# Optimization experiments

Measured on AMD Instinct MI355X. Metric: run time of the kernel, lower is better.

Reference implementation:

```python
import jax, jax.numpy as jnp
import numpy as np

D_IN = 4096
FEATURES = 4096
BATCH = 4096
NUM_ACTIVE = 50
ACTIVE_VAL = 3.0


def _sparse_init(key, shape, num_active=NUM_ACTIVE, active_val=ACTIVE_VAL):
    # Per output column: num_active inputs start ON (active_val), rest OFF (-3.0)
    scores = jax.random.uniform(key, shape)
    k = min(num_active, shape[0])
    threshold = jnp.sort(scores, axis=0)[-k]
    return jnp.where(scores >= threshold[None, :], active_val, -3.0).astype(jnp.float32)


def setup_inputs() -> dict:
    key = jax.random.key(0)
    kx, kw = jax.random.split(key)
    x = jax.random.normal(kx, (BATCH, D_IN), dtype=jnp.float32)
    w_raw = _sparse_init(kw, (D_IN, FEATURES))
    return {"x": x, "w_raw": w_raw}


def reference(x, w_raw):
    # Binary weights via straight-through estimator.
    w_soft = jax.nn.sigmoid(w_raw)
    w_hard = (w_raw > 0.0).astype(jnp.float32)
    w = w_soft + jax.lax.stop_gradient(w_hard - w_soft)
    return x @ w
```

## Files before the change

### kernel.cpp

```cpp
#include <hip/hip_runtime.h>
#include <hip/hip_fp16.h>

#define D_IN 4096
#define FEAT 4096
#define BATCH 4096
#define MAX_SLOTS 64
#define BFEAT 16
#define RCAP 8
#define OVCAP 16

typedef _Float16 h2 __attribute__((ext_vector_type(2)));

__device__ __forceinline__ h2 bc(unsigned u) { return __builtin_bit_cast(h2, u); }

__global__ void scan_kernel(const float* __restrict__ w,
                            unsigned int* __restrict__ c16,
                            unsigned char* __restrict__ rbuf,
                            unsigned int* __restrict__ ocnt,
                            unsigned short* __restrict__ ovf) {
    int t = blockIdx.x * blockDim.x + threadIdx.x;
    float4 v = ((const float4*)w)[t];
    int flat = t * 4;
    float a[4] = {v.x, v.y, v.z, v.w};
#pragma unroll
    for (int c = 0; c < 4; ++c) {
        if (a[c] > 0.0f) {
            int e = flat + c;
            int F = e & (FEAT - 1);
            int i = e >> 12;
            int r = i & 15;
            unsigned int p = atomicAdd(&c16[(F << 4) + r], 1u);
            if (p < RCAP) {
                rbuf[(size_t)((F << 4) + r) * RCAP + p] = (unsigned char)(i >> 4);
            } else {
                unsigned int op = atomicAdd(&ocnt[F], 1u);
                if (op < OVCAP) ovf[(size_t)F * OVCAP + op] = (unsigned short)i;
            }
        }
    }
}

__global__ __launch_bounds__(256)
void emit_kernel(const unsigned int* __restrict__ c16,
                 const unsigned char* __restrict__ rbuf,
                 const unsigned int* __restrict__ ocnt,
                 const unsigned short* __restrict__ ovf,
                 unsigned int* __restrict__ cnt,
                 unsigned short* __restrict__ idx) {
    __shared__ __align__(16) unsigned short outl[BFEAT][MAX_SLOTS];
    __shared__ unsigned short extras[BFEAT][48];
    __shared__ unsigned int   ecnt[BFEAT];
    __shared__ unsigned short kk[BFEAT][16];
    __shared__ unsigned short nn[BFEAT];

    const int tid = threadIdx.x;
    const int f0  = blockIdx.x * BFEAT;
    const int f   = tid >> 4, r = tid & 15;
    const int F   = f0 + f;

    if (tid < BFEAT) ecnt[tid] = 0u;
    __syncthreads();

    unsigned int c = c16[(F << 4) + r];
    int kr = c > RCAP ? RCAP : (int)c;
    kk[f][r] = (unsigned short)kr;
    __syncthreads();

    if (r == 0) {
        int s = 0;
#pragma unroll
        for (int q = 0; q < 16; ++q) s += (int)kk[f][q];
        int ov = (int)ocnt[F]; if (ov > OVCAP) ov = OVCAP;
        s += ov;
        if (s > MAX_SLOTS) s = MAX_SLOTS;
        nn[f] = (unsigned short)s;
        cnt[F] = (unsigned int)s;
    }
    __syncthreads();

    const int n = (int)nn[f];
    uint2 braw = *reinterpret_cast<const uint2*>(rbuf + (size_t)((F << 4) + r) * RCAP);
    const unsigned char* bs = reinterpret_cast<const unsigned char*>(&braw);
    const int base = (r - F) & 15;
    const int tgt  = (n >> 4) + (base < (n & 15) ? 1 : 0);
    const int m    = kr < tgt ? kr : tgt;
    for (int j = 0; j < m; ++j)
        outl[f][base + (j << 4)] = (unsigned short)(((int)bs[j] << 8) | (r << 4));
    for (int j = m; j < kr; ++j) {
        unsigned int e = atomicAdd(&ecnt[f], 1u);
        if (e < 48) extras[f][e] = (unsigned short)(((int)bs[j] << 8) | (r << 4));
    }
    if (r == 0) {
        int ov = (int)ocnt[F]; if (ov > OVCAP) ov = OVCAP;
        for (int j = 0; j < ov; ++j) {
            unsigned int e = atomicAdd(&ecnt[f], 1u);
            if (e < 48) extras[f][e] = (unsigned short)(ovf[(size_t)F * OVCAP + j] << 4);
        }
    }
    __syncthreads();

    if (tid < BFEAT) {
        const int ff = tid, FF = f0 + ff;
        const int n2 = (int)nn[ff];
        int ep = 0, ec = (int)ecnt[ff]; if (ec > 48) ec = 48;
        for (int r2 = 0; r2 < 16 && ep < ec; ++r2) {
            const int b2 = (r2 - FF) & 15;
            const int t2 = (n2 >> 4) + (b2 < (n2 & 15) ? 1 : 0);
            for (int j = (int)kk[ff][r2]; j < t2 && ep < ec; ++j)
                outl[ff][b2 + (j << 4)] = extras[ff][ep++];
        }
    }
    __syncthreads();

    if (tid < BFEAT * 8) {
        const int ff = tid >> 3, o = tid & 7;
        const uint4 v = *reinterpret_cast<const uint4*>(&outl[ff][o << 3]);
        reinterpret_cast<uint4*>(idx)[(size_t)o * FEAT + f0 + ff] = v;
    }
}

__device__ __forceinline__ void do_oct(uint4 p, const char* __restrict__ xtb,
                                       h2& A01, h2& A23, h2& A45, h2& A67,
                                       h2& B01, h2& B23, h2& B45, h2& B67) {
    uint4 v0 = *(const uint4*)(xtb + (p.x & 0xFFF0u));
    uint4 v1 = *(const uint4*)(xtb + (p.x >> 16));
    uint4 v2 = *(const uint4*)(xtb + (p.y & 0xFFF0u));
    uint4 v3 = *(const uint4*)(xtb + (p.y >> 16));
    uint4 v4 = *(const uint4*)(xtb + (p.z & 0xFFF0u));
    uint4 v5 = *(const uint4*)(xtb + (p.z >> 16));
    uint4 v6 = *(const uint4*)(xtb + (p.w & 0xFFF0u));
    uint4 v7 = *(const uint4*)(xtb + (p.w >> 16));
    A01 += bc(v0.x); A23 += bc(v0.y); A45 += bc(v0.z); A67 += bc(v0.w);
    B01 += bc(v1.x); B23 += bc(v1.y); B45 += bc(v1.z); B67 += bc(v1.w);
    A01 += bc(v2.x); A23 += bc(v2.y); A45 += bc(v2.z); A67 += bc(v2.w);
    B01 += bc(v3.x); B23 += bc(v3.y); B45 += bc(v3.z); B67 += bc(v3.w);
    A01 += bc(v4.x); A23 += bc(v4.y); A45 += bc(v4.z); A67 += bc(v4.w);
    B01 += bc(v5.x); B23 += bc(v5.y); B45 += bc(v5.z); B67 += bc(v5.w);
    A01 += bc(v6.x); A23 += bc(v6.y); A45 += bc(v6.z); A67 += bc(v6.w);
    B01 += bc(v7.x); B23 += bc(v7.y); B45 += bc(v7.z); B67 += bc(v7.w);
}

__global__ __launch_bounds__(1024, 8)
void gather_kernel(const float* __restrict__ x,
                   const unsigned int* __restrict__ cnt,
                   const uint4* __restrict__ q,
                   const unsigned short* __restrict__ q16,
                   float* __restrict__ out) {
    __shared__ uint4 xt[D_IN];
    const int tid = threadIdx.x;
    const int b0  = blockIdx.x * 8;
    const float* xb = x + (size_t)b0 * D_IN;

    for (int c = tid; c < D_IN; c += 1024) {
        float r0 = xb[c];
        float r1 = xb[c + D_IN];
        float r2 = xb[c + 2 * D_IN];
        float r3 = xb[c + 3 * D_IN];
        float r4 = xb[c + 4 * D_IN];
        float r5 = xb[c + 5 * D_IN];
        float r6 = xb[c + 6 * D_IN];
        float r7 = xb[c + 7 * D_IN];
        __half2 p01 = __floats2half2_rn(r0, r1);
        __half2 p23 = __floats2half2_rn(r2, r3);
        __half2 p45 = __floats2half2_rn(r4, r5);
        __half2 p67 = __floats2half2_rn(r6, r7);
        uint4 v;
        v.x = *(unsigned*)&p01;
        v.y = *(unsigned*)&p23;
        v.z = *(unsigned*)&p45;
        v.w = *(unsigned*)&p67;
        xt[c] = v;
    }
    __syncthreads();

    const char* xtb = (const char*)xt;

#pragma unroll
    for (int k = 0; k < 4; k += 2) {
        const int fA = tid + k * 1024;
        const int fB = fA + 1024;
        int nA = (int)cnt[fA]; if (nA > MAX_SLOTS) nA = MAX_SLOTS;
        int nB = (int)cnt[fB]; if (nB > MAX_SLOTS) nB = MAX_SLOTS;
        const uint4* qA = q + fA;
        const uint4* qB = q + fB;

        h2 aA01 = {0,0}, aA23 = {0,0}, aA45 = {0,0}, aA67 = {0,0};
        h2 bA01 = {0,0}, bA23 = {0,0}, bA45 = {0,0}, bA67 = {0,0};
        h2 aB01 = {0,0}, aB23 = {0,0}, aB45 = {0,0}, aB67 = {0,0};
        h2 bB01 = {0,0}, bB23 = {0,0}, bB45 = {0,0}, bB67 = {0,0};

        const int nqA = nA >> 3, nqB = nB >> 3;
        const int jm = nqA < nqB ? nqA : nqB;
        if (jm > 0) {
            uint4 pA = qA[0];
            uint4 pB = qB[0];
            for (int j = 0; j < jm; ++j) {
                const int jn = (j + 1 < jm) ? j + 1 : j;
                uint4 nxA = qA[(size_t)jn * FEAT];
                uint4 nxB = qB[(size_t)jn * FEAT];
                do_oct(pA, xtb, aA01, aA23, aA45, aA67, bA01, bA23, bA45, bA67);
                do_oct(pB, xtb, aB01, aB23, aB45, aB67, bB01, bB23, bB45, bB67);
                pA = nxA; pB = nxB;
            }
        }
        for (int j = jm; j < nqA; ++j)
            do_oct(qA[(size_t)j * FEAT], xtb, aA01, aA23, aA45, aA67, bA01, bA23, bA45, bA67);
        for (int j = jm; j < nqB; ++j)
            do_oct(qB[(size_t)j * FEAT], xtb, aB01, aB23, aB45, aB67, bB01, bB23, bB45, bB67);

        {
            int rem = nA & 7;
            int base = (nqA * FEAT + fA) * 8;
            for (int t = 0; t < rem; ++t) {
                uint4 v = *(const uint4*)(xtb + q16[base + t]);
                aA01 += bc(v.x); aA23 += bc(v.y); aA45 += bc(v.z); aA67 += bc(v.w);
            }
        }
        {
            int rem = nB & 7;
            int base = (nqB * FEAT + fB) * 8;
            for (int t = 0; t < rem; ++t) {
                uint4 v = *(const uint4*)(xtb + q16[base + t]);
                aB01 += bc(v.x); aB23 += bc(v.y); aB45 += bc(v.z); aB67 += bc(v.w);
            }
        }

        float* oA = out + fA;
        oA[(size_t)(b0 + 0) * FEAT] = (float)aA01[0] + (float)bA01[0];
        oA[(size_t)(b0 + 1) * FEAT] = (float)aA01[1] + (float)bA01[1];
        oA[(size_t)(b0 + 2) * FEAT] = (float)aA23[0] + (float)bA23[0];
        oA[(size_t)(b0 + 3) * FEAT] = (float)aA23[1] + (float)bA23[1];
        oA[(size_t)(b0 + 4) * FEAT] = (float)aA45[0] + (float)bA45[0];
        oA[(size_t)(b0 + 5) * FEAT] = (float)aA45[1] + (float)bA45[1];
        oA[(size_t)(b0 + 6) * FEAT] = (float)aA67[0] + (float)bA67[0];
        oA[(size_t)(b0 + 7) * FEAT] = (float)aA67[1] + (float)bA67[1];
        float* oB = out + fB;
        oB[(size_t)(b0 + 0) * FEAT] = (float)aB01[0] + (float)bB01[0];
        oB[(size_t)(b0 + 1) * FEAT] = (float)aB01[1] + (float)bB01[1];
        oB[(size_t)(b0 + 2) * FEAT] = (float)aB23[0] + (float)bB23[0];
        oB[(size_t)(b0 + 3) * FEAT] = (float)aB23[1] + (float)bB23[1];
        oB[(size_t)(b0 + 4) * FEAT] = (float)aB45[0] + (float)bB45[0];
        oB[(size_t)(b0 + 5) * FEAT] = (float)aB45[1] + (float)bB45[1];
        oB[(size_t)(b0 + 6) * FEAT] = (float)aB67[0] + (float)bB67[0];
        oB[(size_t)(b0 + 7) * FEAT] = (float)aB67[1] + (float)bB67[1];
    }
}

extern "C" void kernel_launch(void* const* d_in, const int* in_sizes, int n_in,
                              void* d_out, int out_size, void* d_ws, size_t ws_size,
                              hipStream_t stream) {
    const float* x = (const float*)d_in[0];
    const float* w = (const float*)d_in[1];
    float* out = (float*)d_out;

    char* ws = (char*)d_ws;
    unsigned int*   cnt  = (unsigned int*)  (ws);
    unsigned short* idx  = (unsigned short*)(ws + (16u << 10));
    unsigned int*   c16  = (unsigned int*)  (ws + (528u << 10));
    unsigned int*   ocnt = (unsigned int*)  (ws + (784u << 10));
    unsigned char*  rbuf = (unsigned char*) (ws + (800u << 10));
    unsigned short* ovf  = (unsigned short*)(ws + (1312u << 10));

    hipMemsetAsync(c16, 0, (272u << 10), stream);

    scan_kernel<<<(D_IN * FEAT / 4) / 256, 256, 0, stream>>>(w, c16, rbuf, ocnt, ovf);
    emit_kernel<<<FEAT / BFEAT, 256, 0, stream>>>(c16, rbuf, ocnt, ovf, cnt, idx);

    gather_kernel<<<BATCH / 8, 1024, 0, stream>>>(x, cnt, (const uint4*)idx, idx, out);
}
```

Baseline: 229.9 us.

## Vectorize x staging loads and restructure emit slot filling with gap lists

In the gather kernel, each thread now loads float4 vectors from each of the 8 batch rows instead of scalar floats, cutting the number of global load instructions in the x staging phase. The emit kernel is restructured so 128 threads each handle two row-bins, record unfilled slot positions in a shared gap list, and the final fill becomes a direct gap-to-extra copy instead of a nested scan. It also zero-fills unused slots. These are two unrelated changes.

```diff
diff --git a/kernel.cpp b/kernel.cpp
--- a/kernel.cpp
+++ b/kernel.cpp
@@ -49,27 +49,29 @@
                  unsigned short* __restrict__ idx) {
     __shared__ __align__(16) unsigned short outl[BFEAT][MAX_SLOTS];
     __shared__ unsigned short extras[BFEAT][48];
-    __shared__ unsigned int   ecnt[BFEAT];
+    __shared__ unsigned char  gapsl[BFEAT][48];
+    __shared__ unsigned int   ecnt[BFEAT], gcnt[BFEAT];
     __shared__ unsigned short kk[BFEAT][16];
     __shared__ unsigned short nn[BFEAT];
 
     const int tid = threadIdx.x;
     const int f0  = blockIdx.x * BFEAT;
-    const int f   = tid >> 4, r = tid & 15;
-    const int F   = f0 + f;
-
-    if (tid < BFEAT) ecnt[tid] = 0u;
-    __syncthreads();
-
-    unsigned int c = c16[(F << 4) + r];
-    int kr = c > RCAP ? RCAP : (int)c;
-    kk[f][r] = (unsigned short)kr;
-    __syncthreads();
-
-    if (r == 0) {
+
+    if (tid < BFEAT) { ecnt[tid] = 0u; gcnt[tid] = 0u; }
+    __syncthreads();
+
+    {
+        const int f = tid >> 4, r = tid & 15;
+        unsigned int c = c16[((f0 + f) << 4) + r];
+        kk[f][r] = (unsigned short)(c > RCAP ? RCAP : c);
+    }
+    __syncthreads();
+
+    if ((tid & 15) == 0) {
+        const int f = tid >> 4, F = f0 + f;
         int s = 0;
 #pragma unroll
-        for (int q = 0; q < 16; ++q) s += (int)kk[f][q];
+        for (int q2 = 0; q2 < 16; ++q2) s += (int)kk[f][q2];
         int ov = (int)ocnt[F]; if (ov > OVCAP) ov = OVCAP;
         s += ov;
         if (s > MAX_SLOTS) s = MAX_SLOTS;
@@ -78,19 +80,45 @@
     }
     __syncthreads();
 
-    const int n = (int)nn[f];
-    uint2 braw = *reinterpret_cast<const uint2*>(rbuf + (size_t)((F << 4) + r) * RCAP);
-    const unsigned char* bs = reinterpret_cast<const unsigned char*>(&braw);
-    const int base = (r - F) & 15;
-    const int tgt  = (n >> 4) + (base < (n & 15) ? 1 : 0);
-    const int m    = kr < tgt ? kr : tgt;
-    for (int j = 0; j < m; ++j)
-        outl[f][base + (j << 4)] = (unsigned short)(((int)bs[j] << 8) | (r << 4));
-    for (int j = m; j < kr; ++j) {
-        unsigned int e = atomicAdd(&ecnt[f], 1u);
-        if (e < 48) extras[f][e] = (unsigned short)(((int)bs[j] << 8) | (r << 4));
-    }
-    if (r == 0) {
+    if (tid < BFEAT * 8) {
+        const int f = tid >> 3, q = tid & 7;
+        const int F = f0 + f;
+        const int n = (int)nn[f];
+        const int kr0 = (int)kk[f][q], kr1 = (int)kk[f][q + 8];
+        uint2 b0 = *reinterpret_cast<const uint2*>(rbuf + (size_t)((F << 4) + q) * RCAP);
+        uint2 b1 = *reinterpret_cast<const uint2*>(rbuf + (size_t)((F << 4) + q + 8) * RCAP);
+        const unsigned char* s0 = reinterpret_cast<const unsigned char*>(&b0);
+        const unsigned char* s1 = reinterpret_cast<const unsigned char*>(&b1);
+        const int base0 = (q - F) & 15;
+        const int base1 = (q + 8 - F) & 15;
+        const int tgt0 = (n >> 4) + (base0 < (n & 15) ? 1 : 0);
+        const int tgt1 = (n >> 4) + (base1 < (n & 15) ? 1 : 0);
+        const int ni = kr0 + kr1, np = tgt0 + tgt1;
+        const int m = ni < np ? ni : np;
+        for (int t = 0; t < m; ++t) {
+            unsigned short val = (t < kr0)
+                ? (unsigned short)(((int)s0[t] << 8) | (q << 4))
+                : (unsigned short)(((int)s1[t - kr0] << 8) | ((q + 8) << 4));
+            int p = (t < tgt0) ? base0 + (t << 4) : base1 + ((t - tgt0) << 4);
+            outl[f][p] = val;
+        }
+        for (int t = m; t < ni; ++t) {
+            unsigned short val = (t < kr0)
+                ? (unsigned short)(((int)s0[t] << 8) | (q << 4))
+                : (unsigned short)(((int)s1[t - kr0] << 8) | ((q + 8) << 4));
+            unsigned int e = atomicAdd(&ecnt[f], 1u);
+            if (e < 48) extras[f][e] = val;
+        }
+        for (int t = m; t < np; ++t) {
+            int p = (t < tgt0) ? base0 + (t << 4) : base1 + ((t - tgt0) << 4);
+            unsigned int g = atomicAdd(&gcnt[f], 1u);
+            if (g < 48) gapsl[f][g] = (unsigned char)p;
+        }
+        for (int j = tgt0; j < 4; ++j) outl[f][base0 + (j << 4)] = 0;
+        for (int j = tgt1; j < 4; ++j) outl[f][base1 + (j << 4)] = 0;
+    }
+    if (tid < BFEAT) {
+        const int f = tid, F = f0 + f;
         int ov = (int)ocnt[F]; if (ov > OVCAP) ov = OVCAP;
         for (int j = 0; j < ov; ++j) {
             unsigned int e = atomicAdd(&ecnt[f], 1u);
@@ -100,15 +128,12 @@
     __syncthreads();
 
     if (tid < BFEAT) {
-        const int ff = tid, FF = f0 + ff;
-        const int n2 = (int)nn[ff];
-        int ep = 0, ec = (int)ecnt[ff]; if (ec > 48) ec = 48;
-        for (int r2 = 0; r2 < 16 && ep < ec; ++r2) {
-            const int b2 = (r2 - FF) & 15;
-            const int t2 = (n2 >> 4) + (b2 < (n2 & 15) ? 1 : 0);
-            for (int j = (int)kk[ff][r2]; j < t2 && ep < ec; ++j)
-                outl[ff][b2 + (j << 4)] = extras[ff][ep++];
-        }
+        const int f = tid;
+        int g = (int)gcnt[f]; if (g > 48) g = 48;
+        int e = (int)ecnt[f]; if (e > 48) e = 48;
+        const int m2 = g < e ? g : e;
+        for (int t = 0; t < m2; ++t)
+            outl[f][gapsl[f][t]] = extras[f][t];
     }
     __syncthreads();
 
@@ -151,25 +176,31 @@
     const int b0  = blockIdx.x * 8;
     const float* xb = x + (size_t)b0 * D_IN;
 
-    for (int c = tid; c < D_IN; c += 1024) {
-        float r0 = xb[c];
-        float r1 = xb[c + D_IN];
-        float r2 = xb[c + 2 * D_IN];
-        float r3 = xb[c + 3 * D_IN];
-        float r4 = xb[c + 4 * D_IN];
-        float r5 = xb[c + 5 * D_IN];
-        float r6 = xb[c + 6 * D_IN];
-        float r7 = xb[c + 7 * D_IN];
-        __half2 p01 = __floats2half2_rn(r0, r1);
-        __half2 p23 = __floats2half2_rn(r2, r3);
-        __half2 p45 = __floats2half2_rn(r4, r5);
-        __half2 p67 = __floats2half2_rn(r6, r7);
-        uint4 v;
-        v.x = *(unsigned*)&p01;
-        v.y = *(unsigned*)&p23;
-        v.z = *(unsigned*)&p45;
-        v.w = *(unsigned*)&p67;
-        xt[c] = v;
+    {
+        const int c4 = tid << 2;
+        float4 r0 = *(const float4*)(xb + c4);
+        float4 r1 = *(const float4*)(xb + c4 + D_IN);
+        float4 r2 = *(const float4*)(xb + c4 + 2 * D_IN);
+        float4 r3 = *(const float4*)(xb + c4 + 3 * D_IN);
+        float4 r4 = *(const float4*)(xb + c4 + 4 * D_IN);
+        float4 r5 = *(const float4*)(xb + c4 + 5 * D_IN);
+        float4 r6 = *(const float4*)(xb + c4 + 6 * D_IN);
+        float4 r7 = *(const float4*)(xb + c4 + 7 * D_IN);
+#define PACK_COL(cc, comp)                                          \
+        {                                                           \
+            __half2 p01 = __floats2half2_rn(r0.comp, r1.comp);      \
+            __half2 p23 = __floats2half2_rn(r2.comp, r3.comp);      \
+            __half2 p45 = __floats2half2_rn(r4.comp, r5.comp);      \
+            __half2 p67 = __floats2half2_rn(r6.comp, r7.comp);      \
+            uint4 v;                                                \
+            v.x = *(unsigned*)&p01;                                 \
+            v.y = *(unsigned*)&p23;                                 \
+            v.z = *(unsigned*)&p45;                                 \
+            v.w = *(unsigned*)&p67;                                 \
+            xt[c4 + cc] = v;                                        \
+        }
+        PACK_COL(0, x) PACK_COL(1, y) PACK_COL(2, z) PACK_COL(3, w)
+#undef PACK_COL
     }
     __syncthreads();
 
```

New measurement: 206.8 us. 10.0% less time.
